# Optimization experiments

Measured on AMD Instinct MI355X. Metric: run time of the kernel, lower is better.

## Reference

```python
import jax, jax.numpy as jnp
import numpy as np

N_NODES = 100000
NEG_SLOPE = 0.2  # DGL GATConv default negative_slope


def gat_layer(x, src, dst, W, attn_l, attn_r, bias, n_nodes):
    """Single-head DGL GATConv. x: [N, in], returns [N, out]."""
    h = x @ W                              # [N, out]  fc (no bias)
    el = h @ attn_l                        # [N]
    er = h @ attn_r                        # [N]
    e = el[src] + er[dst]                  # [E]
    e = jnp.where(e >= 0, e, NEG_SLOPE * e)  # leaky_relu
    # segment softmax over incoming edges of each dst node
    m = jax.ops.segment_max(e, dst, num_segments=n_nodes)   # [N]
    ex = jnp.exp(e - m[dst])                                 # [E]
    s = jax.ops.segment_sum(ex, dst, num_segments=n_nodes)  # [N]
    a = ex / s[dst]                                          # [E]
    # weighted aggregate of source features
    msg = a[:, None] * h[src]                                # [E, out]
    out = jax.ops.segment_sum(msg, dst, num_segments=n_nodes)
    return out + bias


def setup_inputs() -> dict:
    key = jax.random.key(0)
    ks = jax.random.split(key, 12)
    n, e = N_NODES, 1600000
    in_f, hid_f, out_f = 128, 64, 64
    inp = {
        "features": jax.random.normal(ks[0], (n, in_f), dtype=jnp.float32),
        "edge_weights": jax.random.uniform(ks[1], (e,), dtype=jnp.float32),
        "src": jax.random.randint(ks[2], (e,), 0, n, dtype=jnp.int32),
        "dst": jax.random.randint(ks[3], (e,), 0, n, dtype=jnp.int32),
        "W1": jax.random.normal(ks[4], (in_f, hid_f), dtype=jnp.float32) * (1.0 / np.sqrt(in_f)),
        "attn_l1": jax.random.normal(ks[5], (hid_f,), dtype=jnp.float32) * 0.1,
        "attn_r1": jax.random.normal(ks[6], (hid_f,), dtype=jnp.float32) * 0.1,
        "bias1": jnp.zeros((hid_f,), dtype=jnp.float32),
        "W2": jax.random.normal(ks[7], (hid_f, out_f), dtype=jnp.float32) * (1.0 / np.sqrt(hid_f)),
        "attn_l2": jax.random.normal(ks[8], (out_f,), dtype=jnp.float32) * 0.1,
        "attn_r2": jax.random.normal(ks[9], (out_f,), dtype=jnp.float32) * 0.1,
        "bias2": jnp.zeros((out_f,), dtype=jnp.float32),
    }
    return inp


def reference(features, edge_weights, src, dst, W1, attn_l1, attn_r1, bias1,
              W2, attn_l2, attn_r2, bias2):
    n = features.shape[0]
    # conv1 -> DGL returns [N, 1, hid]; relu; conv2 -> [N, 1, 1, out]
    h = gat_layer(features, src, dst, W1, attn_l1, attn_r1, bias1, n)  # [N, hid]
    h = jax.nn.relu(h)
    out = gat_layer(h, src, dst, W2, attn_l2, attn_r2, bias2, n)       # [N, out]
    # edge_weights is accepted but unused, matching the original forward
    return out.reshape(n, 1, 1, -1)
```

## Files before the change

kernel.cpp:

```cpp
#include <hip/hip_runtime.h>
#include <hip/hip_fp16.h>
#include <type_traits>

#define NEG_SLOPE 0.2f
#define BKT_SHIFT 8
#define BKT_SIZE (1 << BKT_SHIFT)
#define NPB 98
#define NPB_PAD 128
#define SCAP 96
#define BCAP 6144
#define P1_EPT 64

typedef __attribute__((ext_vector_type(8))) short short8;
typedef __attribute__((ext_vector_type(4))) float float4v;

__device__ inline int rfl_i(int v) { return __builtin_amdgcn_readfirstlane(v); }

__device__ inline unsigned short f2bf(float f) {
    unsigned u = __float_as_uint(f);
    unsigned r = u + 0x7FFFu + ((u >> 16) & 1u);
    return (unsigned short)(r >> 16);
}
__device__ inline float bf2f(unsigned short b) {
    return __uint_as_float(((unsigned)b) << 16);
}

__device__ __forceinline__ void partition_body(
        const int* __restrict__ src, const int* __restrict__ dst, int e,
        int* __restrict__ part, int* __restrict__ cnts2, int nbkt,
        int blk, char* smem) {
    int* cnt = (int*)smem;
    int t = threadIdx.x;
    for (int i = t; i < 392; i += 256) cnt[i] = 0;
    __syncthreads();
    int cb = blk * (256 * P1_EPT);
#pragma unroll
    for (int i4 = 0; i4 < P1_EPT / 4; ++i4) {
        int eid0 = cb + (i4 * 256 + t) * 4;
        int4 s4, d4;
        bool full = (eid0 + 3 < e);
        if (full) {
            s4 = *(const int4*)(src + eid0);
            d4 = *(const int4*)(dst + eid0);
        }
#pragma unroll
        for (int j = 0; j < 4; ++j) {
            int eid = eid0 + j;
            int s, d;
            if (full) {
                s = (&s4.x)[j];
                d = (&d4.x)[j];
            } else if (eid < e) {
                s = src[eid];
                d = dst[eid];
            } else {
                continue;
            }
            int b = d >> BKT_SHIFT;
            int r = atomicAdd(&cnt[b], 1);
            if (r < SCAP)
                part[((size_t)b * NPB + blk) * SCAP + r] =
                    (s << BKT_SHIFT) | (d & (BKT_SIZE - 1));
        }
    }
    __syncthreads();
    for (int b = t; b < nbkt; b += 256)
        cnts2[b * NPB_PAD + blk] = min(cnt[b], SCAP);
}

__device__ __forceinline__ void finesort_body(
        const int* __restrict__ part, const int* __restrict__ cnts2,
        int* __restrict__ row_beg, int* __restrict__ row_end,
        int* __restrict__ csr_src, int n, int b, char* smem) {
    int* cnt   = (int*)smem;
    int* cur   = cnt + 256;
    int* tmp   = cur + 256;
    int* soff  = tmp + 256;
    int* rc    = soff + 128;
    int* stage = rc + 128;
    int t = threadIdx.x;
    int c = (t < NPB) ? cnts2[b * NPB_PAD + t] : 0;
    tmp[t] = c;
    if (t < NPB) rc[t] = c;
    __syncthreads();
    for (int o = 1; o < 256; o <<= 1) {
        int x = tmp[t];
        int y = (t >= o) ? tmp[t - o] : 0;
        __syncthreads();
        tmp[t] = x + y;
        __syncthreads();
    }
    if (t < NPB) soff[t] = tmp[t] - c;
    int Seff = min(tmp[255], BCAP);
    __syncthreads();
    int wid = t >> 6, lane = t & 63;
    for (int r = wid; r < NPB; r += 4) {
        int cr = rc[r], orr = soff[r];
        const int* sp = part + ((size_t)b * NPB + r) * SCAP;
        for (int i = lane; i < cr; i += 64) {
            int p = orr + i;
            if (p < BCAP) stage[p] = sp[i];
        }
    }
    cnt[t] = 0;
    __syncthreads();
    for (int i = t; i < Seff; i += 256)
        atomicAdd(&cnt[stage[i] & (BKT_SIZE - 1)], 1);
    __syncthreads();
    int d0 = b << BKT_SHIFT;
    int nloc = min(BKT_SIZE, n - d0);
    int cc = cnt[t];
    tmp[t] = cc;
    __syncthreads();
    for (int o = 1; o < 256; o <<= 1) {
        int x = tmp[t];
        int y = (t >= o) ? tmp[t - o] : 0;
        __syncthreads();
        tmp[t] = x + y;
        __syncthreads();
    }
    int pos0 = b * BCAP + tmp[t] - cc;
    cur[t] = pos0;
    if (t < nloc) {
        row_beg[d0 + t] = pos0;
        row_end[d0 + t] = pos0 + cc;
    }
    __syncthreads();
    for (int i = t; i < Seff; i += 256) {
        int pk = stage[i];
        int pos = atomicAdd(&cur[pk & (BKT_SIZE - 1)], 1);
        csr_src[pos] = ((unsigned)pk) >> BKT_SHIFT;
    }
}

template <int KT, typename IN>
__device__ __forceinline__ void gemm_body(
        const IN* __restrict__ x, const float* __restrict__ W,
        const float* __restrict__ al, const float* __restrict__ ar,
        __half* __restrict__ h16, float* __restrict__ el,
        float* __restrict__ er, int n, int bid, int nblocks,
        int tbeg, int tend, char* smem) {
    constexpr int K = KT * 32;
    constexpr int WFRAG = KT * 4 * 64 * 8;
    unsigned short* Wh = (unsigned short*)smem;
    unsigned short* Wl = Wh + WFRAG;
    for (int idx = threadIdx.x; idx < KT * 4 * 64; idx += 256) {
        int lane = idx & 63, fbkt = idx >> 6;
        int fb = fbkt & 3, kt = fbkt >> 2;
        int q = lane >> 4, c = lane & 15;
#pragma unroll
        for (int j = 0; j < 8; ++j) {
            float w = W[(kt * 32 + q * 8 + j) * 64 + fb * 16 + c];
            unsigned short hi = f2bf(w);
            Wh[idx * 8 + j] = hi;
            Wl[idx * 8 + j] = f2bf(w - bf2f(hi));
        }
    }
    __syncthreads();

    int lane = threadIdx.x & 63;
    int q = lane >> 4, c = lane & 15;
    int wave = bid * 4 + (int)(threadIdx.x >> 6);
    int nwaves = nblocks * 4;
    int ntiles = (n + 15) >> 4;
    if (tend > ntiles) tend = ntiles;

    float alv[4], arv[4];
#pragma unroll
    for (int fb = 0; fb < 4; ++fb) {
        alv[fb] = al[fb * 16 + c];
        arv[fb] = ar[fb * 16 + c];
    }

    for (int t = tbeg + wave; t < tend; t += nwaves) {
        int v0 = t * 16;
        int row = min(v0 + c, n - 1);
        const IN* xr = x + (size_t)row * K + q * 8;

        short8 Ah[KT], Al[KT];
#pragma unroll
        for (int kt = 0; kt < KT; ++kt) {
            float xv[8];
            if constexpr (std::is_same<IN, float>::value) {
                *(float4*)&xv[0] = *(const float4*)(xr + kt * 32);
                *(float4*)&xv[4] = *(const float4*)(xr + kt * 32 + 4);
            } else {
                __half hh[8];
                *(uint4*)hh = *(const uint4*)(xr + kt * 32);
#pragma unroll
                for (int j = 0; j < 8; ++j) xv[j] = __half2float(hh[j]);
            }
#pragma unroll
            for (int j = 0; j < 8; ++j) {
                unsigned short hi = f2bf(xv[j]);
                Ah[kt][j] = (short)hi;
                Al[kt][j] = (short)f2bf(xv[j] - bf2f(hi));
            }
        }

        float4v acc[4];
#pragma unroll
        for (int fb = 0; fb < 4; ++fb) acc[fb] = (float4v)0.f;

#pragma unroll
        for (int kt = 0; kt < KT; ++kt) {
#pragma unroll
            for (int fb = 0; fb < 4; ++fb) {
                short8 bh = *(const short8*)&Wh[((kt * 4 + fb) * 64 + lane) * 8];
                short8 bl = *(const short8*)&Wl[((kt * 4 + fb) * 64 + lane) * 8];
                acc[fb] = __builtin_amdgcn_mfma_f32_16x16x32_bf16(Ah[kt], bh, acc[fb], 0, 0, 0);
                acc[fb] = __builtin_amdgcn_mfma_f32_16x16x32_bf16(Al[kt], bh, acc[fb], 0, 0, 0);
                acc[fb] = __builtin_amdgcn_mfma_f32_16x16x32_bf16(Ah[kt], bl, acc[fb], 0, 0, 0);
            }
        }

#pragma unroll
        for (int r = 0; r < 4; ++r) {
            int v = v0 + q * 4 + r;
            float pl = 0.f, pr = 0.f;
            bool ok = (v < n);
#pragma unroll
            for (int fb = 0; fb < 4; ++fb) {
                float hv = acc[fb][r];
                if (ok) h16[(size_t)v * 64 + fb * 16 + c] = __float2half(hv);
                pl = fmaf(hv, alv[fb], pl);
                pr = fmaf(hv, arv[fb], pr);
            }
#pragma unroll
            for (int off = 8; off > 0; off >>= 1) {
                pl += __shfl_xor(pl, off);
                pr += __shfl_xor(pr, off);
            }
            if (ok && c == 0) { el[v] = pl; er[v] = pr; }
        }
    }
}

__global__ __launch_bounds__(256) void part_gemm1a(
        const int* __restrict__ src, const int* __restrict__ dst, int e,
        int* __restrict__ part, int* __restrict__ cnts2, int nbkt,
        const float* __restrict__ x, const float* __restrict__ W1,
        const float* __restrict__ al, const float* __restrict__ ar,
        __half* __restrict__ h16, float* __restrict__ el,
        float* __restrict__ er, int n, int t1) {
    __shared__ char smem[32768];
    int b = (int)blockIdx.x;
    if (b < NPB)
        partition_body(src, dst, e, part, cnts2, nbkt, b, smem);
    else
        gemm_body<4, float>(x, W1, al, ar, h16, el, er, n, b - NPB, 512,
                            0, t1, smem);
}

__global__ __launch_bounds__(256) void fine_gemm1b(
        const int* __restrict__ part, const int* __restrict__ cnts2,
        int* __restrict__ row_beg, int* __restrict__ row_end,
        int* __restrict__ csr_src, int nbkt,
        const float* __restrict__ x, const float* __restrict__ W1,
        const float* __restrict__ al, const float* __restrict__ ar,
        __half* __restrict__ h16, float* __restrict__ el,
        float* __restrict__ er, int n, int t1) {
    __shared__ char smem[32768];
    int b = (int)blockIdx.x;
    if (b < nbkt)
        finesort_body(part, cnts2, row_beg, row_end, csr_src, n, b, smem);
    else
        gemm_body<4, float>(x, W1, al, ar, h16, el, er, n, b - nbkt, 512,
                            t1, 1 << 30, smem);
}

template <int KT, typename IN>
__global__ __launch_bounds__(256) void gemm_mfma_kernel(
        const IN* __restrict__ x, const float* __restrict__ W,
        const float* __restrict__ al, const float* __restrict__ ar,
        __half* __restrict__ h16, float* __restrict__ el,
        float* __restrict__ er, int n) {
    __shared__ char smem[KT * 4 * 64 * 8 * 2 * 2];
    gemm_body<KT, IN>(x, W, al, ar, h16, el, er, n, (int)blockIdx.x,
                      (int)gridDim.x, 0, 1 << 30, smem);
}

template <typename OUT>
__global__ __launch_bounds__(256) void agg_kernel(
        const int* __restrict__ row_beg, const int* __restrict__ row_end,
        const int* __restrict__ csr_src, const __half* __restrict__ h16,
        const float* __restrict__ el, const float* __restrict__ er,
        const float* __restrict__ bias, OUT* __restrict__ out,
        int n, int do_relu) {
    int lane = threadIdx.x & 63;
    int grp = lane >> 4;
    int c = lane & 15;
    int gwave = rfl_i((int)((blockIdx.x * blockDim.x + threadIdx.x) >> 6));
    int nwaves = (gridDim.x * blockDim.x) >> 6;
    float4 b4 = ((const float4*)bias)[c];
    for (int v = gwave; v < n; v += nwaves) {
        int rs = rfl_i(row_beg[v]), re = rfl_i(row_end[v]);
        float er_v = er[v];
        float a0 = 0.f, a1 = 0.f, a2 = 0.f, a3 = 0.f, ssum = 0.f;
        for (int base = rs; base < re; base += 64) {
            int cnt = min(64, re - base);
            int s_e = 0;
            float ex = 0.f;
            if (lane < cnt) {
                s_e = csr_src[base + lane];
                float ev = el[s_e] + er_v;
                ev = (ev >= 0.f) ? ev : NEG_SLOPE * ev;
                ex = __expf(ev);
            }
            float cs = ex;
#pragma unroll
            for (int off = 32; off > 0; off >>= 1) cs += __shfl_xor(cs, off);
            ssum += cs;
            int cnt16 = (cnt + 15) & ~15;
            for (int j = 0; j < cnt16; j += 16) {
                int sj[4];
                float exj[4];
                uint2 hv[4];
#pragma unroll
                for (int u = 0; u < 4; ++u) {
                    int idx = j + 4 * u + grp;
                    sj[u] = __shfl(s_e, idx);
                    exj[u] = __shfl(ex, idx);
                    hv[u] = *((const uint2*)(h16 + (size_t)sj[u] * 64) + c);
                }
#pragma unroll
                for (int u = 0; u < 4; ++u) {
                    float2 f01 = __half22float2(*(__half2*)&hv[u].x);
                    float2 f23 = __half22float2(*(__half2*)&hv[u].y);
                    a0 = fmaf(exj[u], f01.x, a0);
                    a1 = fmaf(exj[u], f01.y, a1);
                    a2 = fmaf(exj[u], f23.x, a2);
                    a3 = fmaf(exj[u], f23.y, a3);
                }
            }
        }
#pragma unroll
        for (int off = 16; off < 64; off <<= 1) {
            a0 += __shfl_xor(a0, off);
            a1 += __shfl_xor(a1, off);
            a2 += __shfl_xor(a2, off);
            a3 += __shfl_xor(a3, off);
        }
        if (lane < 16) {
            float4 o;
            if (re > rs) {
                float inv = 1.0f / ssum;
                o.x = fmaf(a0, inv, b4.x);
                o.y = fmaf(a1, inv, b4.y);
                o.z = fmaf(a2, inv, b4.z);
                o.w = fmaf(a3, inv, b4.w);
            } else {
                o = b4;
            }
            if (do_relu) {
                o.x = fmaxf(o.x, 0.f);
                o.y = fmaxf(o.y, 0.f);
                o.z = fmaxf(o.z, 0.f);
                o.w = fmaxf(o.w, 0.f);
            }
            if constexpr (std::is_same<OUT, __half>::value) {
                uint2 pk;
                *(__half2*)&pk.x = __float22half2_rn(make_float2(o.x, o.y));
                *(__half2*)&pk.y = __float22half2_rn(make_float2(o.z, o.w));
                ((uint2*)(out + (size_t)v * 64))[c] = pk;
            } else {
                ((float4*)(out + (size_t)v * 64))[c] = o;
            }
        }
    }
}

extern "C" void kernel_launch(void* const* d_in, const int* in_sizes, int n_in,
                              void* d_out, int out_size, void* d_ws, size_t ws_size,
                              hipStream_t stream) {
    (void)n_in; (void)out_size; (void)ws_size;
    const float* features = (const float*)d_in[0];
    const int*   src = (const int*)d_in[2];
    const int*   dst = (const int*)d_in[3];
    const float* W1  = (const float*)d_in[4];
    const float* al1 = (const float*)d_in[5];
    const float* ar1 = (const float*)d_in[6];
    const float* b1  = (const float*)d_in[7];
    const float* W2  = (const float*)d_in[8];
    const float* al2 = (const float*)d_in[9];
    const float* ar2 = (const float*)d_in[10];
    const float* b2  = (const float*)d_in[11];

    const int n = in_sizes[0] / 128;
    const int e = in_sizes[2];
    float* out = (float*)d_out;

    char* p = (char*)d_ws;
    auto alloc = [&](size_t bytes) -> char* {
        char* q = p;
        p += (bytes + 255) & ~(size_t)255;
        return q;
    };
    const int nbkt = (n + BKT_SIZE - 1) >> BKT_SHIFT;

    int*    row_beg = (int*)alloc((size_t)n * 4);
    int*    row_end = (int*)alloc((size_t)n * 4);
    int*    csr_src = (int*)alloc((size_t)nbkt * BCAP * 4);
    __half* h16     = (__half*)alloc((size_t)n * 64 * 2);
    __half* hr      = (__half*)alloc((size_t)n * 64 * 2);
    float*  el      = (float*)alloc((size_t)n * 4);
    float*  er      = (float*)alloc((size_t)n * 4);
    int*    cnts2   = (int*)alloc((size_t)nbkt * NPB_PAD * 4);
    int*    part    = (int*)alloc((size_t)nbkt * NPB * SCAP * 4);

    const int ntiles = (n + 15) >> 4;
    const int t1 = (ntiles * 2) / 5;

    part_gemm1a<<<NPB + 512, 256, 0, stream>>>(src, dst, e, part, cnts2, nbkt,
                                               features, W1, al1, ar1,
                                               h16, el, er, n, t1);
    fine_gemm1b<<<nbkt + 512, 256, 0, stream>>>(part, cnts2, row_beg, row_end,
                                                csr_src, nbkt,
                                                features, W1, al1, ar1,
                                                h16, el, er, n, t1);
    agg_kernel<__half><<<4096, 256, 0, stream>>>(row_beg, row_end, csr_src, h16,
                                                 el, er, b1, hr, n, 1);
    gemm_mfma_kernel<2, __half><<<512, 256, 0, stream>>>(hr, W2, al2, ar2,
                                                         h16, el, er, n);
    agg_kernel<float><<<4096, 256, 0, stream>>>(row_beg, row_end, csr_src, h16,
                                                el, er, b2, out, n, 0);
}
```

Before: 249.0 us.

## Split edge partitioning across more blocks and rework fine-sort staging copy

Raises the number of partition blocks from 98 to 391 with fewer edges per thread and smaller per-slot capacity, which spreads the bucketing pass over more workgroups. The fine-sort stage now has each thread own two partition slots and copy them serially, replacing the wave-per-slot copy loop, and it drops the soff/rc shared arrays. The GEMM split between the two fused kernels moves to half the tiles each, and the aggregation grids shrink to 2048 blocks. Risks include overflowing the smaller SCAP=48 slot capacity, which would drop edges, and uncoalesced serial per-thread copies in fine-sort.

```diff
diff --git a/kernel.cpp b/kernel.cpp
--- a/kernel.cpp
+++ b/kernel.cpp
@@ -5,11 +5,11 @@
 #define NEG_SLOPE 0.2f
 #define BKT_SHIFT 8
 #define BKT_SIZE (1 << BKT_SHIFT)
-#define NPB 98
-#define NPB_PAD 128
-#define SCAP 96
+#define NPB 391
+#define NPB_PAD 400
+#define SCAP 48
 #define BCAP 6144
-#define P1_EPT 64
+#define P1_EPT 16
 
 typedef __attribute__((ext_vector_type(8))) short short8;
 typedef __attribute__((ext_vector_type(4))) float float4v;
@@ -75,13 +75,13 @@
     int* cnt   = (int*)smem;
     int* cur   = cnt + 256;
     int* tmp   = cur + 256;
-    int* soff  = tmp + 256;
-    int* rc    = soff + 128;
-    int* stage = rc + 128;
+    int* stage = tmp + 256;
     int t = threadIdx.x;
-    int c = (t < NPB) ? cnts2[b * NPB_PAD + t] : 0;
-    tmp[t] = c;
-    if (t < NPB) rc[t] = c;
+    int blk0 = 2 * t, blk1 = 2 * t + 1;
+    int c0 = (blk0 < NPB) ? cnts2[b * NPB_PAD + blk0] : 0;
+    int c1 = (blk1 < NPB) ? cnts2[b * NPB_PAD + blk1] : 0;
+    int s = c0 + c1;
+    tmp[t] = s;
     __syncthreads();
     for (int o = 1; o < 256; o <<= 1) {
         int x = tmp[t];
@@ -90,16 +90,19 @@
         tmp[t] = x + y;
         __syncthreads();
     }
-    if (t < NPB) soff[t] = tmp[t] - c;
+    int excl = tmp[t] - s;
     int Seff = min(tmp[255], BCAP);
-    __syncthreads();
-    int wid = t >> 6, lane = t & 63;
-    for (int r = wid; r < NPB; r += 4) {
-        int cr = rc[r], orr = soff[r];
-        const int* sp = part + ((size_t)b * NPB + r) * SCAP;
-        for (int i = lane; i < cr; i += 64) {
-            int p = orr + i;
-            if (p < BCAP) stage[p] = sp[i];
+    {
+        const int* sp0 = part + ((size_t)b * NPB + blk0) * SCAP;
+        for (int i = 0; i < c0; ++i) {
+            int p = excl + i;
+            if (p < BCAP) stage[p] = sp0[i];
+        }
+        const int* sp1 = part + ((size_t)b * NPB + blk1) * SCAP;
+        int sb1 = excl + c0;
+        for (int i = 0; i < c1; ++i) {
+            int p = sb1 + i;
+            if (p < BCAP) stage[p] = sp1[i];
         }
     }
     cnt[t] = 0;
@@ -409,7 +412,7 @@
     int*    part    = (int*)alloc((size_t)nbkt * NPB * SCAP * 4);
 
     const int ntiles = (n + 15) >> 4;
-    const int t1 = (ntiles * 2) / 5;
+    const int t1 = ntiles / 2;
 
     part_gemm1a<<<NPB + 512, 256, 0, stream>>>(src, dst, e, part, cnts2, nbkt,
                                                features, W1, al1, ar1,
@@ -418,10 +421,10 @@
                                                 csr_src, nbkt,
                                                 features, W1, al1, ar1,
                                                 h16, el, er, n, t1);
-    agg_kernel<__half><<<4096, 256, 0, stream>>>(row_beg, row_end, csr_src, h16,
+    agg_kernel<__half><<<2048, 256, 0, stream>>>(row_beg, row_end, csr_src, h16,
                                                  el, er, b1, hr, n, 1);
     gemm_mfma_kernel<2, __half><<<512, 256, 0, stream>>>(hr, W2, al2, ar2,
                                                          h16, el, er, n);
-    agg_kernel<float><<<4096, 256, 0, stream>>>(row_beg, row_end, csr_src, h16,
+    agg_kernel<float><<<2048, 256, 0, stream>>>(row_beg, row_end, csr_src, h16,
                                                 el, er, b2, out, n, 0);
 }
```

Measured after the change: 244.3 us (median of 2 runs). Within noise of the previous version (-1.9%).
